# Kernel optimization log

Hardware: AMD Instinct MI355X
Metric: run time of the kernel (lower is better)

The kernel has to match this reference:

```python
import jax, jax.numpy as jnp
import numpy as np

B, S, E, H = 4, 1024, 1024, 16
D = E // H  # head_dim


def setup_inputs() -> dict:
    key = jax.random.key(0)
    ks = jax.random.split(key, 12)
    s = 1.0 / np.sqrt(E)
    return {
        "value": jax.random.normal(ks[0], (B, S, E), jnp.float32),
        "key_in": jax.random.normal(ks[1], (B, S, E), jnp.float32),
        "query": jax.random.normal(ks[2], (B, S, E), jnp.float32),
        "mask": jax.random.randint(ks[3], (B, 1, 1, S), 0, 2, jnp.int32),
        "Wq": jax.random.normal(ks[4], (E, E), jnp.float32) * s,
        "bq": jnp.zeros((E,), jnp.float32),
        "Wk": jax.random.normal(ks[5], (E, E), jnp.float32) * s,
        "bk": jnp.zeros((E,), jnp.float32),
        "Wv": jax.random.normal(ks[6], (E, E), jnp.float32) * s,
        "bv": jnp.zeros((E,), jnp.float32),
        "Wo": jax.random.normal(ks[7], (E, E), jnp.float32) * s,
        "bo": jnp.zeros((E,), jnp.float32),
    }


def reference(value, key_in, query, mask, Wq, bq, Wk, bk, Wv, bv, Wo, bo):
    b = query.shape[0]
    # torch Linear: y = x @ W.T + b
    Q = (query @ Wq.T + bq).reshape(b, query.shape[1], H, D)
    K = (key_in @ Wk.T + bk).reshape(b, key_in.shape[1], H, D)
    V = (value @ Wv.T + bv).reshape(b, value.shape[1], H, D)
    # scores scaled by 1/sqrt(embed_dim) (faithful to source, not head_dim)
    energy = jnp.einsum("bqhd,bkhd->bhqk", Q, K) / jnp.sqrt(jnp.float32(E))
    energy = jnp.where(mask == 0, jnp.float32(-1e20), energy)
    attention = jax.nn.softmax(energy, axis=-1)
    out = jnp.einsum("bhqk,bkhd->bqhd", attention, V).reshape(b, query.shape[1], E)
    return out @ Wo.T + bo
```

## Files before the change

### kernel.cpp

```cpp
#include <hip/hip_runtime.h>


typedef unsigned short u16;
typedef __bf16 bf16x8 __attribute__((ext_vector_type(8)));
typedef __bf16 bf16x2 __attribute__((ext_vector_type(2)));
typedef short s16x4 __attribute__((ext_vector_type(4)));
typedef float f32x4 __attribute__((ext_vector_type(4)));
typedef float f32x16 __attribute__((ext_vector_type(16)));

struct alignas(8) us4_t { u16 x, y, z, w; };

__device__ __forceinline__ u16 f2bf(float x) {
  unsigned int u = __builtin_bit_cast(unsigned int, x);
  unsigned int r = u + 0x7fffu + ((u >> 16) & 1u);
  return (u16)(r >> 16);
}

__device__ __forceinline__ unsigned int pack2bf(float a, float b) {
#if __has_builtin(__builtin_amdgcn_cvt_pk_bf16_f32)
  bf16x2 r = __builtin_amdgcn_cvt_pk_bf16_f32(a, b);
  return __builtin_bit_cast(unsigned int, r);
#else
  return (unsigned int)f2bf(a) | ((unsigned int)f2bf(b) << 16);
#endif
}

__device__ __forceinline__ f32x4 zero4() {
  f32x4 z; z[0] = 0.f; z[1] = 0.f; z[2] = 0.f; z[3] = 0.f; return z;
}

__device__ __forceinline__ void async_copy16(const void* g, void* l) {
  __builtin_amdgcn_global_load_lds(
      (__attribute__((address_space(1))) void*)(uintptr_t)g,
      (__attribute__((address_space(3))) void*)l, 16, 0, 0);
}

__global__ void fused_cast(const float* __restrict__ q, const float* __restrict__ k,
                           const float* __restrict__ v, const float* __restrict__ wq,
                           const float* __restrict__ wk, const float* __restrict__ wv,
                           const float* __restrict__ wo, const int* __restrict__ mask,
                           u16* __restrict__ qo, u16* __restrict__ ko, u16* __restrict__ vo,
                           u16* __restrict__ wqo, u16* __restrict__ wko, u16* __restrict__ wvo,
                           u16* __restrict__ woo, float* __restrict__ biasf) {
  const int blk = blockIdx.x;
  if (blk >= 16384) {
    int i = (blk - 16384) * 256 + threadIdx.x;
    biasf[i] = mask[i] ? 0.f : -1.4427e20f;
    return;
  }
  const float* src; u16* dst; int off;
  if (blk < 4096)       { src = q;  dst = qo;  off = blk; }
  else if (blk < 8192)  { src = k;  dst = ko;  off = blk - 4096; }
  else if (blk < 12288) { src = v;  dst = vo;  off = blk - 8192; }
  else if (blk < 13312) { src = wq; dst = wqo; off = blk - 12288; }
  else if (blk < 14336) { src = wk; dst = wko; off = blk - 13312; }
  else if (blk < 15360) { src = wv; dst = wvo; off = blk - 14336; }
  else                  { src = wo; dst = woo; off = blk - 15360; }
  const size_t i = (size_t)off * 256 + threadIdx.x;
  float4 f = ((const float4*)src)[i];
  unsigned int lo = pack2bf(f.x, f.y), hi = pack2bf(f.z, f.w);
  unsigned long long pk = (unsigned long long)lo | ((unsigned long long)hi << 32);
  ((unsigned long long*)dst)[i] = pk;
}

template <bool OUT_BF16, int NT>
__device__ __forceinline__ void gemm_core32(const u16* __restrict__ A,
                                            const u16* __restrict__ Bw,
                                            const float* __restrict__ bias,
                                            void* __restrict__ outp, bool trans,
                                            int m0, int n0) {
  __shared__ u16 lA[128 * 64];
  __shared__ u16 lB[NT * 64 * 64];
  const int tid = threadIdx.x;
  const int lane = tid & 63, w = tid >> 6;
  const int wm = w >> 1, wn = w & 1;
  const int l32 = lane & 31, hi = lane >> 5;
  const int rg = lane >> 3, cs = lane & 7;

  f32x16 acc[2][NT];
#pragma unroll
  for (int i = 0; i < 2; ++i)
#pragma unroll
    for (int j = 0; j < NT; ++j)
#pragma unroll
      for (int e = 0; e < 16; ++e) acc[i][j][e] = 0.f;

  for (int it = 0; it < 16; ++it) {
    const int k0 = it * 64;
#pragma unroll
    for (int t = 0; t < 4; ++t) {
      const int row = w * 32 + t * 8 + rg;
      const int c = cs ^ (row & 7);
      async_copy16(A + (size_t)(m0 + row) * 1024 + k0 + c * 8, &lA[(w * 32 + t * 8) * 64]);
    }
#pragma unroll
    for (int t = 0; t < NT * 2; ++t) {
      const int row = w * (NT * 16) + t * 8 + rg;
      const int c = cs ^ (row & 7);
      async_copy16(Bw + (size_t)(n0 + row) * 1024 + k0 + c * 8,
                   &lB[(w * (NT * 16) + t * 8) * 64]);
    }
    __syncthreads();
#pragma unroll
    for (int s = 0; s < 4; ++s) {
      bf16x8 af[2], bfr[NT];
#pragma unroll
      for (int i = 0; i < 2; ++i) {
        const int row = wm * 64 + i * 32 + l32;
        af[i] = *(const bf16x8*)&lA[row * 64 + (((s * 2 + hi) ^ (row & 7)) * 8)];
      }
#pragma unroll
      for (int j = 0; j < NT; ++j) {
        const int row = wn * (NT * 32) + j * 32 + l32;
        bfr[j] = *(const bf16x8*)&lB[row * 64 + (((s * 2 + hi) ^ (row & 7)) * 8)];
      }
#pragma unroll
      for (int i = 0; i < 2; ++i)
#pragma unroll
        for (int j = 0; j < NT; ++j)
          acc[i][j] = __builtin_amdgcn_mfma_f32_32x32x16_bf16(af[i], bfr[j], acc[i][j], 0, 0, 0);
    }
    __syncthreads();
  }

#pragma unroll
  for (int j = 0; j < NT; ++j) {
    const int cg = n0 + wn * (NT * 32) + j * 32 + l32;
    const float bj = bias[cg];
#pragma unroll
    for (int i = 0; i < 2; ++i) {
      const int mbase = m0 + wm * 64 + i * 32 + 4 * hi;
#pragma unroll
      for (int g = 0; g < 4; ++g) {
        const int r0 = mbase + 8 * g;
        if (!trans) {
          if (OUT_BF16) {
            u16* o = (u16*)outp;
#pragma unroll
            for (int rr = 0; rr < 4; ++rr)
              o[(size_t)(r0 + rr) * 1024 + cg] = f2bf(acc[i][j][g * 4 + rr] + bj);
          } else {
            float* o = (float*)outp;
#pragma unroll
            for (int rr = 0; rr < 4; ++rr)
              o[(size_t)(r0 + rr) * 1024 + cg] = acc[i][j][g * 4 + rr] + bj;
          }
        } else {
          u16* o = (u16*)outp;
          const int bh = ((r0 >> 10) << 4) + (cg >> 6);
          const int g2 = (r0 & 1023) >> 2;
          const int d  = cg & 63;
          union { us4_t s; unsigned int u[2]; } pk;
          pk.u[0] = pack2bf(acc[i][j][g * 4 + 0] + bj, acc[i][j][g * 4 + 1] + bj);
          pk.u[1] = pack2bf(acc[i][j][g * 4 + 2] + bj, acc[i][j][g * 4 + 3] + bj);
          *(us4_t*)&o[(size_t)bh * 65536 + g2 * 256 + d * 4] = pk.s;
        }
      }
    }
  }
}

__global__ __launch_bounds__(256, 3) void qkv_gemm(
    const u16* __restrict__ Xq, const u16* __restrict__ Xk, const u16* __restrict__ Xv,
    const u16* __restrict__ Wq, const u16* __restrict__ Wk, const u16* __restrict__ Wv,
    const float* __restrict__ bq, const float* __restrict__ bk, const float* __restrict__ bv,
    u16* __restrict__ Qo, u16* __restrict__ Ko, u16* __restrict__ Vto) {
  const int flat = blockIdx.x;
  const int xcd = flat & 7, t = flat >> 3;
  const int n = t & 7, bandl = t >> 3;
  const int band = xcd * 12 + bandl;
  const int z = band >> 5, m = band & 31;
  const u16* A = (z == 0) ? Xq : (z == 1) ? Xk : Xv;
  const u16* W = (z == 0) ? Wq : (z == 1) ? Wk : Wv;
  const float* bias = (z == 0) ? bq : (z == 1) ? bk : bv;
  u16* out = (z == 0) ? Qo : (z == 1) ? Ko : Vto;
  gemm_core32<true, 2>(A, W, bias, out, z == 2, m * 128, n * 128);
}

__global__ __launch_bounds__(256, 2) void out_gemm(
    const u16* __restrict__ A, const u16* __restrict__ W,
    const float* __restrict__ bias, float* __restrict__ out) {
  const int flat = blockIdx.x;
  const int xcd = flat & 7, t = flat >> 3;
  const int n = t & 15, m = xcd * 4 + (t >> 4);
  gemm_core32<false, 1>(A, W, bias, out, false, m * 128, n * 64);
}

__global__ __launch_bounds__(256, 4) void attn_kernel(
    const u16* __restrict__ Qb, const u16* __restrict__ Kb, const u16* __restrict__ Vtb,
    const float* __restrict__ biasf, u16* __restrict__ Ob) {
  __shared__ u16 lK[128 * 64];
  __shared__ u16 lV[64 * 128];
  u16* lQ = lV;

  const int tid = threadIdx.x;
  const int lane = tid & 63, w = tid >> 6;
  const int quad = lane >> 4, l16 = lane & 15;
  const int rg = lane >> 3, cs = lane & 7;

  const int flat = blockIdx.x;
  const int xcd = flat & 7, r = flat >> 3;
  const int bh = xcd * 8 + (r & 7), qt = r >> 3;
  const int b = bh >> 4;
  const size_t qkBase = (size_t)b * 1048576 + (size_t)(bh & 15) * 64;
  const size_t vBase = (size_t)bh * 65536;
  const float C = 0.0450842200277982f;
  const float* bp = biasf + b * 1024 + quad * 4;

#pragma unroll
  for (int t = 0; t < 2; ++t) {
    const int row = w * 16 + t * 8 + rg;
    const int c = cs ^ (row & 7);
    async_copy16(Qb + qkBase + (size_t)(qt * 64 + row) * 1024 + c * 8,
                 &lQ[(w * 16 + t * 8) * 64]);
  }
  __syncthreads();

  bf16x8 qf[2];
#pragma unroll
  for (int kk = 0; kk < 2; ++kk) {
    const int row = w * 16 + l16;
    qf[kk] = *(const bf16x8*)&lQ[row * 64 + (((kk * 4 + quad) ^ (row & 7)) * 8)];
  }
  __syncthreads();

  float lsum = 0.f;
  f32x4 oacc[4];
#pragma unroll
  for (int dt = 0; dt < 4; ++dt) oacc[dt] = zero4();

  for (int it = 0; it < 8; ++it) {
    const int k0 = it * 128;
#pragma unroll
    for (int t = 0; t < 4; ++t) {
      const int row = w * 32 + t * 8 + rg;
      const int c = cs ^ (row & 7);
      async_copy16(Kb + qkBase + (size_t)(k0 + row) * 1024 + c * 8,
                   &lK[(w * 32 + t * 8) * 64]);
    }
#pragma unroll
    for (int t = 0; t < 4; ++t) {
      const int o16 = (w * 4 + t) * 512 + lane * 8;
      async_copy16(Vtb + vBase + (size_t)it * 8192 + o16, &lV[(w * 4 + t) * 512]);
    }
    __syncthreads();

    f32x4 sacc[8];
#pragma unroll
    for (int n = 0; n < 8; ++n) sacc[n] = zero4();
#pragma unroll
    for (int kk = 0; kk < 2; ++kk) {
#pragma unroll
      for (int n = 0; n < 8; ++n) {
        const int row = n * 16 + l16;
        bf16x8 kf = *(const bf16x8*)&lK[row * 64 + (((kk * 4 + quad) ^ (row & 7)) * 8)];
        sacc[n] = __builtin_amdgcn_mfma_f32_16x16x32_bf16(kf, qf[kk], sacc[n], 0, 0, 0);
      }
    }

    f32x4 sum4 = zero4();
#pragma unroll
    for (int n = 0; n < 8; ++n) {
      const float4 vb = *(const float4*)&bp[k0 + n * 16];
      sacc[n][0] = __builtin_amdgcn_exp2f(fmaf(sacc[n][0], C, vb.x));
      sacc[n][1] = __builtin_amdgcn_exp2f(fmaf(sacc[n][1], C, vb.y));
      sacc[n][2] = __builtin_amdgcn_exp2f(fmaf(sacc[n][2], C, vb.z));
      sacc[n][3] = __builtin_amdgcn_exp2f(fmaf(sacc[n][3], C, vb.w));
      sum4[0] += sacc[n][0]; sum4[1] += sacc[n][1];
      sum4[2] += sacc[n][2]; sum4[3] += sacc[n][3];
    }
    float rs = (sum4[0] + sum4[1]) + (sum4[2] + sum4[3]);
    rs += __shfl_xor(rs, 16);
    rs += __shfl_xor(rs, 32);
    lsum += rs;

    s16x4 pf[8];
#pragma unroll
    for (int n = 0; n < 8; ++n) {
      union { s16x4 v; unsigned int u[2]; } pu;
      pu.u[0] = pack2bf(sacc[n][0], sacc[n][1]);
      pu.u[1] = pack2bf(sacc[n][2], sacc[n][3]);
      pf[n] = pu.v;
    }

#pragma unroll
    for (int dt = 0; dt < 4; ++dt) {
      const int dbase = (dt * 16 + l16) * 4;
#pragma unroll
      for (int ks = 0; ks < 8; ++ks) {
        s16x4 vf = *(const s16x4*)&lV[(ks * 4 + quad) * 256 + dbase];
        oacc[dt] = __builtin_amdgcn_mfma_f32_16x16x16bf16_1k(vf, pf[ks], oacc[dt], 0, 0, 0);
      }
    }
    __syncthreads();
  }

  const float inv = 1.f / lsum;
  const int qg = qt * 64 + w * 16 + l16;
#pragma unroll
  for (int dt = 0; dt < 4; ++dt) {
    union { us4_t s; unsigned int u[2]; } pk;
    pk.u[0] = pack2bf(oacc[dt][0] * inv, oacc[dt][1] * inv);
    pk.u[1] = pack2bf(oacc[dt][2] * inv, oacc[dt][3] * inv);
    *(us4_t*)&Ob[qkBase + (size_t)qg * 1024 + dt * 16 + quad * 4] = pk.s;
  }
}

extern "C" void kernel_launch(void* const* d_in, const int* in_sizes, int n_in,
                              void* d_out, int out_size, void* d_ws, size_t ws_size,
                              hipStream_t stream) {
  const float* value  = (const float*)d_in[0];
  const float* key_in = (const float*)d_in[1];
  const float* query  = (const float*)d_in[2];
  const int*   mask   = (const int*)d_in[3];
  const float* Wq = (const float*)d_in[4];
  const float* bq = (const float*)d_in[5];
  const float* Wk = (const float*)d_in[6];
  const float* bk = (const float*)d_in[7];
  const float* Wv = (const float*)d_in[8];
  const float* bv = (const float*)d_in[9];
  const float* Wo = (const float*)d_in[10];
  const float* bo = (const float*)d_in[11];

  u16* ws = (u16*)d_ws;
  u16* q_bf  = ws;
  u16* k_bf  = ws + 4194304;
  u16* v_bf  = ws + 8388608;
  u16* wq_bf = ws + 12582912;
  u16* wk_bf = ws + 13631488;
  u16* wv_bf = ws + 14680064;
  u16* wo_bf = ws + 15728640;
  u16* Qbuf  = ws + 16777216;
  u16* Kbuf  = ws + 20971520;
  u16* Vtbuf = ws + 25165824;
  u16* attnb = ws + 29360128;
  float* biasf = (float*)d_out;

  fused_cast<<<16400, 256, 0, stream>>>(query, key_in, value, Wq, Wk, Wv, Wo, mask,
                                        q_bf, k_bf, v_bf, wq_bf, wk_bf, wv_bf, wo_bf,
                                        biasf);
  qkv_gemm<<<dim3(768), 256, 0, stream>>>(q_bf, k_bf, v_bf, wq_bf, wk_bf, wv_bf,
                                          bq, bk, bv, Qbuf, Kbuf, Vtbuf);
  attn_kernel<<<dim3(1024), 256, 0, stream>>>(Qbuf, Kbuf, Vtbuf, biasf, attnb);
  out_gemm<<<dim3(512), 256, 0, stream>>>(attnb, wo_bf, bo, (float*)d_out);
}
```

Baseline: 203.3 us.

## Split-K output GEMM with atomics and register-prefetch K/V in attention

Measured after the change: 291.2 us. 1.43x slower.

```diff
diff --git a/kernel.cpp b/kernel.cpp
--- a/kernel.cpp
+++ b/kernel.cpp
@@ -39,10 +39,17 @@
                            const float* __restrict__ v, const float* __restrict__ wq,
                            const float* __restrict__ wk, const float* __restrict__ wv,
                            const float* __restrict__ wo, const int* __restrict__ mask,
+                           const float* __restrict__ bo,
                            u16* __restrict__ qo, u16* __restrict__ ko, u16* __restrict__ vo,
                            u16* __restrict__ wqo, u16* __restrict__ wko, u16* __restrict__ wvo,
-                           u16* __restrict__ woo, float* __restrict__ biasf) {
+                           u16* __restrict__ woo, float* __restrict__ biasf,
+                           float* __restrict__ dout) {
   const int blk = blockIdx.x;
+  if (blk >= 16400) {
+    const int r = blk - 16400;
+    ((float4*)dout)[r * 256 + threadIdx.x] = ((const float4*)bo)[threadIdx.x];
+    return;
+  }
   if (blk >= 16384) {
     int i = (blk - 16384) * 256 + threadIdx.x;
     biasf[i] = mask[i] ? 0.f : -1.4427e20f;
@@ -63,12 +70,12 @@
   ((unsigned long long*)dst)[i] = pk;
 }
 
-template <bool OUT_BF16, int NT>
+template <bool OUT_BF16, int NT, bool ATOMIC>
 __device__ __forceinline__ void gemm_core32(const u16* __restrict__ A,
                                             const u16* __restrict__ Bw,
                                             const float* __restrict__ bias,
                                             void* __restrict__ outp, bool trans,
-                                            int m0, int n0) {
+                                            int m0, int n0, int it0, int itN) {
   __shared__ u16 lA[128 * 64];
   __shared__ u16 lB[NT * 64 * 64];
   const int tid = threadIdx.x;
@@ -85,7 +92,7 @@
 #pragma unroll
       for (int e = 0; e < 16; ++e) acc[i][j][e] = 0.f;
 
-  for (int it = 0; it < 16; ++it) {
+  for (int it = it0; it < itN; ++it) {
     const int k0 = it * 64;
 #pragma unroll
     for (int t = 0; t < 4; ++t) {
@@ -126,14 +133,20 @@
 #pragma unroll
   for (int j = 0; j < NT; ++j) {
     const int cg = n0 + wn * (NT * 32) + j * 32 + l32;
-    const float bj = bias[cg];
+    float bj = 0.f;
+    if (!ATOMIC) bj = bias[cg];
 #pragma unroll
     for (int i = 0; i < 2; ++i) {
       const int mbase = m0 + wm * 64 + i * 32 + 4 * hi;
 #pragma unroll
       for (int g = 0; g < 4; ++g) {
         const int r0 = mbase + 8 * g;
-        if (!trans) {
+        if (ATOMIC) {
+          float* o = (float*)outp;
+#pragma unroll
+          for (int rr = 0; rr < 4; ++rr)
+            unsafeAtomicAdd(&o[(size_t)(r0 + rr) * 1024 + cg], acc[i][j][g * 4 + rr]);
+        } else if (!trans) {
           if (OUT_BF16) {
             u16* o = (u16*)outp;
 #pragma unroll
@@ -174,16 +187,18 @@
   const u16* W = (z == 0) ? Wq : (z == 1) ? Wk : Wv;
   const float* bias = (z == 0) ? bq : (z == 1) ? bk : bv;
   u16* out = (z == 0) ? Qo : (z == 1) ? Ko : Vto;
-  gemm_core32<true, 2>(A, W, bias, out, z == 2, m * 128, n * 128);
-}
-
-__global__ __launch_bounds__(256, 2) void out_gemm(
+  gemm_core32<true, 2, false>(A, W, bias, out, z == 2, m * 128, n * 128, 0, 16);
+}
+
+__global__ __launch_bounds__(256, 4) void out_gemm(
     const u16* __restrict__ A, const u16* __restrict__ W,
-    const float* __restrict__ bias, float* __restrict__ out) {
+    float* __restrict__ out) {
   const int flat = blockIdx.x;
   const int xcd = flat & 7, t = flat >> 3;
-  const int n = t & 15, m = xcd * 4 + (t >> 4);
-  gemm_core32<false, 1>(A, W, bias, out, false, m * 128, n * 64);
+  const int kh = t & 1, s = t >> 1;
+  const int n = s & 15, m = xcd * 4 + (s >> 4);
+  gemm_core32<false, 1, true>(A, W, nullptr, out, false, m * 128, n * 64,
+                              kh * 8, kh * 8 + 8);
 }
 
 __global__ __launch_bounds__(256, 4) void attn_kernel(
@@ -197,6 +212,7 @@
   const int lane = tid & 63, w = tid >> 6;
   const int quad = lane >> 4, l16 = lane & 15;
   const int rg = lane >> 3, cs = lane & 7;
+  const int c = cs ^ (rg & 7);
 
   const int flat = blockIdx.x;
   const int xcd = flat & 7, r = flat >> 3;
@@ -209,9 +225,7 @@
 
 #pragma unroll
   for (int t = 0; t < 2; ++t) {
-    const int row = w * 16 + t * 8 + rg;
-    const int c = cs ^ (row & 7);
-    async_copy16(Qb + qkBase + (size_t)(qt * 64 + row) * 1024 + c * 8,
+    async_copy16(Qb + qkBase + (size_t)(qt * 64 + w * 16 + t * 8 + rg) * 1024 + c * 8,
                  &lQ[(w * 16 + t * 8) * 64]);
   }
   __syncthreads();
@@ -222,7 +236,15 @@
     const int row = w * 16 + l16;
     qf[kk] = *(const bf16x8*)&lQ[row * 64 + (((kk * 4 + quad) ^ (row & 7)) * 8)];
   }
-  __syncthreads();
+
+  const u16* kSrc = Kb + qkBase + (size_t)(w * 32 + rg) * 1024 + c * 8;
+  const u16* vSrc = Vtb + vBase + (w * 4) * 512 + lane * 8;
+
+  uint4 kpre[4], vpre[4];
+#pragma unroll
+  for (int t = 0; t < 4; ++t) kpre[t] = *(const uint4*)(kSrc + (size_t)(t * 8) * 1024);
+#pragma unroll
+  for (int t = 0; t < 4; ++t) vpre[t] = *(const uint4*)(vSrc + t * 512);
 
   float lsum = 0.f;
   f32x4 oacc[4];
@@ -231,18 +253,20 @@
 
   for (int it = 0; it < 8; ++it) {
     const int k0 = it * 128;
-#pragma unroll
-    for (int t = 0; t < 4; ++t) {
-      const int row = w * 32 + t * 8 + rg;
-      const int c = cs ^ (row & 7);
-      async_copy16(Kb + qkBase + (size_t)(k0 + row) * 1024 + c * 8,
-                   &lK[(w * 32 + t * 8) * 64]);
-    }
-#pragma unroll
-    for (int t = 0; t < 4; ++t) {
-      const int o16 = (w * 4 + t) * 512 + lane * 8;
-      async_copy16(Vtb + vBase + (size_t)it * 8192 + o16, &lV[(w * 4 + t) * 512]);
-    }
+    __syncthreads();
+#pragma unroll
+    for (int t = 0; t < 4; ++t)
+      *(uint4*)&lK[(w * 32 + t * 8 + rg) * 64 + cs * 8] = kpre[t];
+#pragma unroll
+    for (int t = 0; t < 4; ++t)
+      *(uint4*)&lV[(w * 4 + t) * 512 + lane * 8] = vpre[t];
+    const int nit = (it < 7) ? it + 1 : 7;
+#pragma unroll
+    for (int t = 0; t < 4; ++t)
+      kpre[t] = *(const uint4*)(kSrc + (size_t)(nit * 128 + t * 8) * 1024);
+#pragma unroll
+    for (int t = 0; t < 4; ++t)
+      vpre[t] = *(const uint4*)(vSrc + (size_t)nit * 8192 + t * 512);
     __syncthreads();
 
     f32x4 sacc[8];
@@ -269,10 +293,6 @@
       sum4[0] += sacc[n][0]; sum4[1] += sacc[n][1];
       sum4[2] += sacc[n][2]; sum4[3] += sacc[n][3];
     }
-    float rs = (sum4[0] + sum4[1]) + (sum4[2] + sum4[3]);
-    rs += __shfl_xor(rs, 16);
-    rs += __shfl_xor(rs, 32);
-    lsum += rs;
 
     s16x4 pf[8];
 #pragma unroll
@@ -292,7 +312,11 @@
         oacc[dt] = __builtin_amdgcn_mfma_f32_16x16x16bf16_1k(vf, pf[ks], oacc[dt], 0, 0, 0);
       }
     }
-    __syncthreads();
+
+    float rs = (sum4[0] + sum4[1]) + (sum4[2] + sum4[3]);
+    rs += __shfl_xor(rs, 16);
+    rs += __shfl_xor(rs, 32);
+    lsum += rs;
   }
 
   const float inv = 1.f / lsum;
@@ -333,14 +357,14 @@
   u16* Qbuf  = ws + 16777216;
   u16* Kbuf  = ws + 20971520;
   u16* Vtbuf = ws + 25165824;
-  u16* attnb = ws + 29360128;
-  float* biasf = (float*)d_out;
-
-  fused_cast<<<16400, 256, 0, stream>>>(query, key_in, value, Wq, Wk, Wv, Wo, mask,
-                                        q_bf, k_bf, v_bf, wq_bf, wk_bf, wv_bf, wo_bf,
-                                        biasf);
+  u16* attnb = q_bf;
+  float* biasf = (float*)(ws + 29360128);
+
+  fused_cast<<<20496, 256, 0, stream>>>(query, key_in, value, Wq, Wk, Wv, Wo, mask,
+                                        bo, q_bf, k_bf, v_bf, wq_bf, wk_bf, wv_bf,
+                                        wo_bf, biasf, (float*)d_out);
   qkv_gemm<<<dim3(768), 256, 0, stream>>>(q_bf, k_bf, v_bf, wq_bf, wk_bf, wv_bf,
                                           bq, bk, bv, Qbuf, Kbuf, Vtbuf);
   attn_kernel<<<dim3(1024), 256, 0, stream>>>(Qbuf, Kbuf, Vtbuf, biasf, attnb);
-  out_gemm<<<dim3(512), 256, 0, stream>>>(attnb, wo_bf, bo, (float*)d_out);
-}
+  out_gemm<<<dim3(1024), 256, 0, stream>>>(attnb, wo_bf, (float*)d_out);
+}
```

## Fuse fp32-to-bf16 activation cast into QKV GEMM loads

Applied to the files above, without the earlier changes.

Result: slower. 223.1 us (+9.8%).

```diff
diff --git a/kernel.cpp b/kernel.cpp
--- a/kernel.cpp
+++ b/kernel.cpp
@@ -35,27 +35,23 @@
       (__attribute__((address_space(3))) void*)l, 16, 0, 0);
 }
 
-__global__ void fused_cast(const float* __restrict__ q, const float* __restrict__ k,
-                           const float* __restrict__ v, const float* __restrict__ wq,
-                           const float* __restrict__ wk, const float* __restrict__ wv,
-                           const float* __restrict__ wo, const int* __restrict__ mask,
-                           u16* __restrict__ qo, u16* __restrict__ ko, u16* __restrict__ vo,
-                           u16* __restrict__ wqo, u16* __restrict__ wko, u16* __restrict__ wvo,
-                           u16* __restrict__ woo, float* __restrict__ biasf) {
+__global__ void fused_cast(const float* __restrict__ wq, const float* __restrict__ wk,
+                           const float* __restrict__ wv, const float* __restrict__ wo,
+                           const int* __restrict__ mask,
+                           u16* __restrict__ wqo, u16* __restrict__ wko,
+                           u16* __restrict__ wvo, u16* __restrict__ woo,
+                           float* __restrict__ biasf) {
   const int blk = blockIdx.x;
-  if (blk >= 16384) {
-    int i = (blk - 16384) * 256 + threadIdx.x;
+  if (blk >= 4096) {
+    int i = (blk - 4096) * 256 + threadIdx.x;
     biasf[i] = mask[i] ? 0.f : -1.4427e20f;
     return;
   }
   const float* src; u16* dst; int off;
-  if (blk < 4096)       { src = q;  dst = qo;  off = blk; }
-  else if (blk < 8192)  { src = k;  dst = ko;  off = blk - 4096; }
-  else if (blk < 12288) { src = v;  dst = vo;  off = blk - 8192; }
-  else if (blk < 13312) { src = wq; dst = wqo; off = blk - 12288; }
-  else if (blk < 14336) { src = wk; dst = wko; off = blk - 13312; }
-  else if (blk < 15360) { src = wv; dst = wvo; off = blk - 14336; }
-  else                  { src = wo; dst = woo; off = blk - 15360; }
+  if (blk < 1024)       { src = wq; dst = wqo; off = blk; }
+  else if (blk < 2048)  { src = wk; dst = wko; off = blk - 1024; }
+  else if (blk < 3072)  { src = wv; dst = wvo; off = blk - 2048; }
+  else                  { src = wo; dst = woo; off = blk - 3072; }
   const size_t i = (size_t)off * 256 + threadIdx.x;
   float4 f = ((const float4*)src)[i];
   unsigned int lo = pack2bf(f.x, f.y), hi = pack2bf(f.z, f.w);
@@ -63,8 +59,8 @@
   ((unsigned long long*)dst)[i] = pk;
 }
 
-template <bool OUT_BF16, int NT>
-__device__ __forceinline__ void gemm_core32(const u16* __restrict__ A,
+template <bool OUT_BF16, int NT, bool AFP32>
+__device__ __forceinline__ void gemm_core32(const void* __restrict__ Ap,
                                             const u16* __restrict__ Bw,
                                             const float* __restrict__ bias,
                                             void* __restrict__ outp, bool trans,
@@ -87,11 +83,29 @@
 
   for (int it = 0; it < 16; ++it) {
     const int k0 = it * 64;
-#pragma unroll
-    for (int t = 0; t < 4; ++t) {
-      const int row = w * 32 + t * 8 + rg;
-      const int c = cs ^ (row & 7);
-      async_copy16(A + (size_t)(m0 + row) * 1024 + k0 + c * 8, &lA[(w * 32 + t * 8) * 64]);
+    if (AFP32) {
+      const float* Af = (const float*)Ap;
+#pragma unroll
+      for (int t = 0; t < 4; ++t) {
+        const int row = w * 32 + t * 8 + rg;
+        const int c = cs ^ (row & 7);
+        const float* p = Af + (size_t)(m0 + row) * 1024 + k0 + c * 8;
+        float4 f0 = *(const float4*)p;
+        float4 f1 = *(const float4*)(p + 4);
+        uint4 pk;
+        pk.x = pack2bf(f0.x, f0.y); pk.y = pack2bf(f0.z, f0.w);
+        pk.z = pack2bf(f1.x, f1.y); pk.w = pack2bf(f1.z, f1.w);
+        *(uint4*)&lA[row * 64 + cs * 8] = pk;
+      }
+    } else {
+      const u16* Au = (const u16*)Ap;
+#pragma unroll
+      for (int t = 0; t < 4; ++t) {
+        const int row = w * 32 + t * 8 + rg;
+        const int c = cs ^ (row & 7);
+        async_copy16(Au + (size_t)(m0 + row) * 1024 + k0 + c * 8,
+                     &lA[(w * 32 + t * 8) * 64]);
+      }
     }
 #pragma unroll
     for (int t = 0; t < NT * 2; ++t) {
@@ -161,7 +175,7 @@
 }
 
 __global__ __launch_bounds__(256, 3) void qkv_gemm(
-    const u16* __restrict__ Xq, const u16* __restrict__ Xk, const u16* __restrict__ Xv,
+    const float* __restrict__ Xq, const float* __restrict__ Xk, const float* __restrict__ Xv,
     const u16* __restrict__ Wq, const u16* __restrict__ Wk, const u16* __restrict__ Wv,
     const float* __restrict__ bq, const float* __restrict__ bk, const float* __restrict__ bv,
     u16* __restrict__ Qo, u16* __restrict__ Ko, u16* __restrict__ Vto) {
@@ -170,11 +184,11 @@
   const int n = t & 7, bandl = t >> 3;
   const int band = xcd * 12 + bandl;
   const int z = band >> 5, m = band & 31;
-  const u16* A = (z == 0) ? Xq : (z == 1) ? Xk : Xv;
+  const float* A = (z == 0) ? Xq : (z == 1) ? Xk : Xv;
   const u16* W = (z == 0) ? Wq : (z == 1) ? Wk : Wv;
   const float* bias = (z == 0) ? bq : (z == 1) ? bk : bv;
   u16* out = (z == 0) ? Qo : (z == 1) ? Ko : Vto;
-  gemm_core32<true, 2>(A, W, bias, out, z == 2, m * 128, n * 128);
+  gemm_core32<true, 2, true>(A, W, bias, out, z == 2, m * 128, n * 128);
 }
 
 __global__ __launch_bounds__(256, 2) void out_gemm(
@@ -183,7 +197,7 @@
   const int flat = blockIdx.x;
   const int xcd = flat & 7, t = flat >> 3;
   const int n = t & 15, m = xcd * 4 + (t >> 4);
-  gemm_core32<false, 1>(A, W, bias, out, false, m * 128, n * 64);
+  gemm_core32<false, 1, false>(A, W, bias, out, false, m * 128, n * 64);
 }
 
 __global__ __launch_bounds__(256, 4) void attn_kernel(
@@ -269,10 +283,6 @@
       sum4[0] += sacc[n][0]; sum4[1] += sacc[n][1];
       sum4[2] += sacc[n][2]; sum4[3] += sacc[n][3];
     }
-    float rs = (sum4[0] + sum4[1]) + (sum4[2] + sum4[3]);
-    rs += __shfl_xor(rs, 16);
-    rs += __shfl_xor(rs, 32);
-    lsum += rs;
 
     s16x4 pf[8];
 #pragma unroll
@@ -292,6 +302,11 @@
         oacc[dt] = __builtin_amdgcn_mfma_f32_16x16x16bf16_1k(vf, pf[ks], oacc[dt], 0, 0, 0);
       }
     }
+
+    float rs = (sum4[0] + sum4[1]) + (sum4[2] + sum4[3]);
+    rs += __shfl_xor(rs, 16);
+    rs += __shfl_xor(rs, 32);
+    lsum += rs;
     __syncthreads();
   }
 
@@ -323,9 +338,6 @@
   const float* bo = (const float*)d_in[11];
 
   u16* ws = (u16*)d_ws;
-  u16* q_bf  = ws;
-  u16* k_bf  = ws + 4194304;
-  u16* v_bf  = ws + 8388608;
   u16* wq_bf = ws + 12582912;
   u16* wk_bf = ws + 13631488;
   u16* wv_bf = ws + 14680064;
@@ -333,13 +345,12 @@
   u16* Qbuf  = ws + 16777216;
   u16* Kbuf  = ws + 20971520;
   u16* Vtbuf = ws + 25165824;
-  u16* attnb = ws + 29360128;
+  u16* attnb = ws;
   float* biasf = (float*)d_out;
 
-  fused_cast<<<16400, 256, 0, stream>>>(query, key_in, value, Wq, Wk, Wv, Wo, mask,
-                                        q_bf, k_bf, v_bf, wq_bf, wk_bf, wv_bf, wo_bf,
-                                        biasf);
-  qkv_gemm<<<dim3(768), 256, 0, stream>>>(q_bf, k_bf, v_bf, wq_bf, wk_bf, wv_bf,
+  fused_cast<<<4112, 256, 0, stream>>>(Wq, Wk, Wv, Wo, mask,
+                                       wq_bf, wk_bf, wv_bf, wo_bf, biasf);
+  qkv_gemm<<<dim3(768), 256, 0, stream>>>(query, key_in, value, wq_bf, wk_bf, wv_bf,
                                           bq, bk, bv, Qbuf, Kbuf, Vtbuf);
   attn_kernel<<<dim3(1024), 256, 0, stream>>>(Qbuf, Kbuf, Vtbuf, biasf, attnb);
   out_gemm<<<dim3(512), 256, 0, stream>>>(attnb, wo_bf, bo, (float*)d_out);
```
